# Optimization experiments

Hardware: AMD Instinct MI355X
Metric: run time of the kernel (lower is better)

Reference implementation:

```python
import jax, jax.numpy as jnp
import numpy as np

NP_CONST = 48.0  # Np in the original code


def dft_matrices(freq=48, time=512):
    # A[t, f] = exp(-2j*pi*t*f/time)/sqrt(time), split into re/im, shape [time, freq]
    t = np.arange(time)[:, None]
    f = np.arange(freq)[None, :]
    ang = -2.0 * np.pi * t * f / time
    scale = 1.0 / np.sqrt(time)
    return (np.cos(ang) * scale).astype(np.float32), (np.sin(ang) * scale).astype(np.float32)


def _mm(xr, xi, wr, wi):
    # complex matmul: (xr + i xi) @ (wr + i wi)
    return xr @ wr - xi @ wi, xr @ wi + xi @ wr


def _act(R, sigma, theta):
    # scaled soft-threshold (standard LAMP shrinkage); returns f and df/dR
    lam = theta[0] * sigma
    mag = jnp.abs(R)
    shr = jnp.maximum(mag - lam, 0.0)
    f = theta[1] * jnp.sign(R) * shr
    df = theta[1] * (mag > lam).astype(R.dtype)
    return f, df


def setup_inputs() -> dict:
    key = jax.random.key(0)
    L, B = 8, 8192
    dre, dim = dft_matrices(48, 512)
    u = jax.random.normal(key, (B, 48, 2), dtype=jnp.float32)
    # per-layer params initialized to the DFT matrices (as in LAMP_layer.__init__)
    A_re = jnp.broadcast_to(jnp.asarray(dre), (L, 512, 48)).copy()
    A_im = jnp.broadcast_to(jnp.asarray(dim), (L, 512, 48)).copy()
    theta = jnp.broadcast_to(jnp.array([1.0, 1.0, -1.0], dtype=jnp.float32), (L, 3)).copy()
    return {"u": u, "A_re": A_re, "A_im": A_im, "theta": theta,
            "DFT_re": jnp.asarray(dre), "DFT_im": jnp.asarray(dim)}


def _lamp_forward(u, A_re, A_im, theta, DFT_re, DFT_im):
    u_re, u_im = u[:, :, 0], u[:, :, 1]          # [B, 48]
    B = u_re.shape[0]
    z_re, z_im = u_re, u_im
    H_re = jnp.zeros((B, 512), dtype=u.dtype)
    H_im = jnp.zeros((B, 512), dtype=u.dtype)

    def layer(carry, params):
        z_re, z_im, H_re, H_im = carry
        Are, Aim, th = params                      # [512,48], [512,48], [3]
        # Z = z @ A.T : [B,48] x [48,512]
        Z_re, Z_im = _mm(z_re, z_im, Are.T, Aim.T)
        R_re = H_re + Z_re
        R_im = H_im + Z_im
        sigma = jnp.sqrt(jnp.sum(z_re * z_re) + jnp.sum(z_im * z_im)) / jnp.sqrt(NP_CONST)
        Hn_re, d_re = _act(R_re, sigma, th)
        Hn_im, d_im = _act(R_im, sigma, th)
        b_re = d_re.sum() / NP_CONST
        b_im = d_im.sum() / NP_CONST
        # h_hat = H_hat @ A : [B,512] x [512,48]
        h_re, h_im = _mm(Hn_re, Hn_im, Are, Aim)
        zn_re = u_re - h_re + b_re * z_re
        zn_im = u_im - h_im + b_im * z_im
        return (zn_re, zn_im, Hn_re, Hn_im), None

    (z_re, z_im, H_re, H_im), _ = jax.lax.scan(layer, (z_re, z_im, H_re, H_im),
                                               (A_re, A_im, theta))
    h_re, h_im = _mm(H_re, H_im, DFT_re, DFT_im)   # [B, 48]
    return jnp.stack((h_re, h_im), axis=2)          # [B, 48, 2]


def reference(u, A_re, A_im, theta, DFT_re, DFT_im):
    return _lamp_forward(u, A_re, A_im, theta, DFT_re, DFT_im)
```

## Files before the change

kernel.cpp:

```cpp
#include <hip/hip_runtime.h>
#include <hip/hip_bf16.h>
#include <math.h>

#define B_   8192
#define F_   48
#define T_   512
#define L_   8
#define NBLK 256
#define THR  512
#define NW   8
#define RPB  32
#define HST  520
#define ZS   52
#define LINE 32
#define EVT_DW (NBLK * LINE)
#define NEVT 8
#define SYNC_DW (NEVT * EVT_DW)

typedef unsigned short ushort_t;
typedef unsigned int   uint_t;
typedef __attribute__((ext_vector_type(8))) short short8;
typedef __attribute__((ext_vector_type(4))) float f32x4;

#define MFMA(a,b,c) __builtin_amdgcn_mfma_f32_16x16x32_bf16(a,b,c,0,0,0)

__device__ inline ushort_t f2bf(float x) {
    __hip_bfloat16 h = __float2bfloat16(x);
    return *reinterpret_cast<ushort_t*>(&h);
}
__device__ inline short8 negbf(short8 v) {
    short8 r;
    #pragma unroll
    for (int i = 0; i < 8; ++i) r[i] = v[i] ^ (short)0x8000;
    return r;
}
__device__ inline short8 pack8(float4 a, float4 b) {
    short8 r;
    r[0]=(short)f2bf(a.x); r[1]=(short)f2bf(a.y); r[2]=(short)f2bf(a.z); r[3]=(short)f2bf(a.w);
    r[4]=(short)f2bf(b.x); r[5]=(short)f2bf(b.y); r[6]=(short)f2bf(b.z); r[7]=(short)f2bf(b.w);
    return r;
}

__device__ inline float aload(const float* p) {
    return __hip_atomic_load(p, __ATOMIC_RELAXED, __HIP_MEMORY_SCOPE_AGENT);
}
__device__ inline void astore(float* p, float v) {
    __hip_atomic_store(p, v, __ATOMIC_RELAXED, __HIP_MEMORY_SCOPE_AGENT);
}

__device__ inline void publish(float* evtbase, int blk, const float* v, int nv) {
    float* line = evtbase + (size_t)blk * LINE;
    #pragma unroll
    for (int j = 0; j < 8; ++j)
        if (j < nv) astore(line + 1 + j, v[j]);
    __hip_atomic_store((uint_t*)line, 1u, __ATOMIC_RELEASE, __HIP_MEMORY_SCOPE_AGENT);
}

__device__ inline void evt_wait(float* evtbase, int wave, int lane, int nv, float* red) {
    if (wave == 0) {
        uint_t* f0 = (uint_t*)evtbase;
        for (;;) {
            bool ok = true;
            #pragma unroll
            for (int g = 0; g < NBLK / 64; ++g) {
                uint_t fl = __hip_atomic_load(f0 + (size_t)(g * 64 + lane) * LINE,
                                              __ATOMIC_RELAXED, __HIP_MEMORY_SCOPE_AGENT);
                ok = ok && (fl != 0u);
            }
            if (__all(ok)) break;
            __builtin_amdgcn_s_sleep(1);
        }
    }
    __syncthreads();
    if (wave < nv) {
        float s = 0.f;
        #pragma unroll
        for (int g = 0; g < NBLK / 64; ++g)
            s += aload(evtbase + (size_t)(g * 64 + lane) * LINE + 1 + wave);
        #pragma unroll
        for (int o = 32; o > 0; o >>= 1) s += __shfl_xor(s, o, 64);
        if (lane == 0) red[wave] = s;
    }
    __syncthreads();
}

__global__ __launch_bounds__(256) void k_pre(
    const float* __restrict__ Ar, const float* __restrict__ Ai,
    const float* __restrict__ Dr, const float* __restrict__ Di,
    ushort_t* __restrict__ Afr, ushort_t* __restrict__ Afi,
    ushort_t* __restrict__ Atr, ushort_t* __restrict__ Ati,
    ushort_t* __restrict__ Dfr, ushort_t* __restrict__ Dfi,
    uint_t* __restrict__ syncbuf)
{
    const int gt = blockIdx.x * 256 + threadIdx.x;
    const int gs = gridDim.x * 256;
    for (int idx = gt; idx < SYNC_DW; idx += gs) syncbuf[idx] = 0u;
    for (int idx = gt; idx < L_ * 32768; idx += gs) {
        int j = idx & 7, rest = idx >> 3;
        int mm = rest & 15; rest >>= 4;
        int qq = rest & 3;  rest >>= 2;
        int k2 = rest & 1;  rest >>= 1;
        int tile = rest & 31;
        int l = rest >> 5;
        int t = tile * 16 + mm, k = k2 * 32 + qq * 8 + j;
        float vr = 0.f, vi = 0.f;
        if (k < 48) { int g = l * 24576 + t * 48 + k; vr = Ar[g]; vi = Ai[g]; }
        Afr[idx] = f2bf(vr); Afi[idx] = f2bf(vi);
    }
    for (int idx = gt; idx < L_ * 24576; idx += gs) {
        int j = idx & 7, rest = idx >> 3;
        int mm = rest & 15; rest >>= 4;
        int qq = rest & 3;  rest >>= 2;
        int ks = rest & 15; rest >>= 4;
        int ft = rest % 3;
        int l = rest / 3;
        int f = ft * 16 + mm, k = ks * 32 + qq * 8 + j;
        int g = l * 24576 + k * 48 + f;
        Atr[idx] = f2bf(Ar[g]); Ati[idx] = f2bf(Ai[g]);
    }
    for (int idx = gt; idx < 24576; idx += gs) {
        int j = idx & 7, rest = idx >> 3;
        int mm = rest & 15; rest >>= 4;
        int qq = rest & 3;  rest >>= 2;
        int ks = rest & 15;
        int ft = rest >> 4;
        int f = ft * 16 + mm, k = ks * 32 + qq * 8 + j;
        Dfr[idx] = f2bf(Dr[k * 48 + f]); Dfi[idx] = f2bf(Di[k * 48 + f]);
    }
}

__global__ __launch_bounds__(THR, 2) void k_lamp(
    const float* __restrict__ u,
    const ushort_t* __restrict__ Afr, const ushort_t* __restrict__ Afi,
    const ushort_t* __restrict__ Atr, const ushort_t* __restrict__ Ati,
    const ushort_t* __restrict__ Dfr, const ushort_t* __restrict__ Dfi,
    const float* __restrict__ th,
    uint_t* syncbuf,
    float* __restrict__ out)
{
    extern __shared__ char dyn[];
    float*    pR   = (float*)dyn;
    float*    pI   = pR + 8 * 3 * 16 * 17;
    float*    zreL = pI + 8 * 3 * 16 * 17;
    float*    zimL = zreL + RPB * ZS;
    float*    red  = zimL + RPB * ZS;
    ushort_t* HreL = (ushort_t*)(red + 128);
    ushort_t* HimL = HreL + RPB * HST;

    float* evt = (float*)syncbuf;

    const int tid = threadIdx.x, blk = blockIdx.x;
    const int row0 = blk * RPB;
    const int wave = tid >> 6, lane = tid & 63;
    const int quad = lane >> 4, m = lane & 15;
    const int rows16 = (wave >> 2) * 16;
    const int rt = wave >> 2, kq = wave & 3;
    const float2* u2 = (const float2*)u;

    f32x4 hR[8], hI[8];
    #pragma unroll
    for (int ct = 0; ct < 8; ++ct) { hR[ct] = (f32x4){0,0,0,0}; hI[ct] = (f32x4){0,0,0,0}; }

    float acc = 0.f;
    #pragma unroll
    for (int k3 = 0; k3 < 3; ++k3) {
        int j = tid + k3 * THR;
        int r = j / 48, c = j - r * 48;
        float2 v = u2[(row0 + r) * 48 + c];
        zreL[r * ZS + c] = v.x; zimL[r * ZS + c] = v.y;
        acc += v.x * v.x + v.y * v.y;
    }
    #pragma unroll
    for (int o = 32; o > 0; o >>= 1) acc += __shfl_xor(acc, o, 64);
    __syncthreads();
    if (lane == 0) red[16 + wave] = acc;
    __syncthreads();
    if (tid == 0) {
        float t = 0.f;
        #pragma unroll
        for (int w = 0; w < NW; ++w) t += red[16 + w];
        publish(evt, blk, &t, 1);
    }

    float lam = 0.f;
    for (int l = 0; l < L_; ++l) {
        const float th1 = th[l * 3 + 1];

        const float* zpr = zreL + (rows16 + m) * ZS;
        const float* zpi = zimL + (rows16 + m) * ZS;
        short8 zr0 = pack8(*(const float4*)(zpr + quad * 8), *(const float4*)(zpr + quad * 8 + 4));
        short8 zi0 = pack8(*(const float4*)(zpi + quad * 8), *(const float4*)(zpi + quad * 8 + 4));
        short8 zr1 = {0,0,0,0,0,0,0,0}, zi1 = {0,0,0,0,0,0,0,0};
        if (quad < 2) {
            zr1 = pack8(*(const float4*)(zpr + 32 + quad * 8), *(const float4*)(zpr + 36 + quad * 8));
            zi1 = pack8(*(const float4*)(zpi + 32 + quad * 8), *(const float4*)(zpi + 36 + quad * 8));
        }
        short8 zin0 = negbf(zi0), zin1 = negbf(zi1);

        const ushort_t* Aflr = Afr + (size_t)l * 32768;
        const ushort_t* Afli = Afi + (size_t)l * 32768;
        #pragma unroll
        for (int ct = 0; ct < 8; ++ct) {
            const int tile = (wave & 3) * 8 + ct;
            const ushort_t* rp = Aflr + (size_t)(tile * 2) * 512 + lane * 8;
            const ushort_t* ip = Afli + (size_t)(tile * 2) * 512 + lane * 8;
            short8 ar0 = *(const short8*)rp;
            short8 ar1 = *(const short8*)(rp + 512);
            short8 ai0 = *(const short8*)ip;
            short8 ai1 = *(const short8*)(ip + 512);
            hR[ct] = MFMA(zr0, ar0, hR[ct]);
            hR[ct] = MFMA(zr1, ar1, hR[ct]);
            hR[ct] = MFMA(zin0, ai0, hR[ct]);
            hR[ct] = MFMA(zin1, ai1, hR[ct]);
            hI[ct] = MFMA(zr0, ai0, hI[ct]);
            hI[ct] = MFMA(zr1, ai1, hI[ct]);
            hI[ct] = MFMA(zi0, ar0, hI[ct]);
            hI[ct] = MFMA(zi1, ar1, hI[ct]);
        }

        if (l == 0) {
            evt_wait(evt, wave, lane, 1, red);
            lam = th[0] * sqrtf(red[0] * (1.0f / 48.0f));
        }

        float cr = 0.f, ci = 0.f;
        #pragma unroll
        for (int ct = 0; ct < 8; ++ct) {
            const int t = ((wave & 3) * 8 + ct) * 16 + m;
            #pragma unroll
            for (int reg = 0; reg < 4; ++reg) {
                const int lr = rows16 + quad * 4 + reg;
                float Rr = hR[ct][reg], Ri = hI[ct][reg];
                float mr = fabsf(Rr), mi = fabsf(Ri);
                float fr = th1 * copysignf(fmaxf(mr - lam, 0.f), Rr);
                float fi = th1 * copysignf(fmaxf(mi - lam, 0.f), Ri);
                cr += (mr > lam) ? 1.f : 0.f;
                ci += (mi > lam) ? 1.f : 0.f;
                hR[ct][reg] = fr; hI[ct][reg] = fi;
                HreL[lr * HST + t] = f2bf(fr);
                HimL[lr * HST + t] = f2bf(fi);
            }
        }

        if (l == L_ - 1) { __syncthreads(); break; }
        __syncthreads();

        const ushort_t* Atlr = Atr + (size_t)l * 24576;
        const ushort_t* Atli = Ati + (size_t)l * 24576;
        f32x4 aR[3], aI[3];
        #pragma unroll
        for (int q = 0; q < 3; ++q) { aR[q] = (f32x4){0,0,0,0}; aI[q] = (f32x4){0,0,0,0}; }
        #pragma unroll
        for (int ks = 0; ks < 4; ++ks) {
            const int ksa = kq * 4 + ks;
            const int k0 = ksa * 32 + quad * 8;
            short8 hr = *(const short8*)&HreL[(rt * 16 + m) * HST + k0];
            short8 hi = *(const short8*)&HimL[(rt * 16 + m) * HST + k0];
            short8 hin = negbf(hi);
            #pragma unroll
            for (int ft = 0; ft < 3; ++ft) {
                short8 br = *(const short8*)(Atlr + (size_t)((ft * 16 + ksa) * 64 + lane) * 8);
                short8 bi = *(const short8*)(Atli + (size_t)((ft * 16 + ksa) * 64 + lane) * 8);
                aR[ft] = MFMA(hr, br, aR[ft]);
                aR[ft] = MFMA(hin, bi, aR[ft]);
                aI[ft] = MFMA(hr, bi, aI[ft]);
                aI[ft] = MFMA(hi, br, aI[ft]);
            }
        }
        #pragma unroll
        for (int ft = 0; ft < 3; ++ft) {
            #pragma unroll
            for (int reg = 0; reg < 4; ++reg) {
                pR[((wave * 3 + ft) * 16 + quad * 4 + reg) * 17 + m] = aR[ft][reg];
                pI[((wave * 3 + ft) * 16 + quad * 4 + reg) * 17 + m] = aI[ft][reg];
            }
        }
        __syncthreads();

        float aRe[3], aIm[3], zR3[3], zI3[3];
        float S1 = 0.f, S2 = 0.f, S3 = 0.f, S4 = 0.f, S5 = 0.f, S6 = 0.f;
        #pragma unroll
        for (int k3 = 0; k3 < 3; ++k3) {
            int j = tid + k3 * THR;
            int r = j / 48, f = j - r * 48;
            int rt2 = r >> 4, lr = r & 15, ft = f >> 4, c = f & 15;
            float hRv = 0.f, hIv = 0.f;
            #pragma unroll
            for (int q = 0; q < 4; ++q) {
                hRv += pR[(((rt2 * 4 + q) * 3 + ft) * 16 + lr) * 17 + c];
                hIv += pI[(((rt2 * 4 + q) * 3 + ft) * 16 + lr) * 17 + c];
            }
            float2 uv = u2[(row0 + r) * 48 + f];
            float zr = zreL[r * ZS + f], zi = zimL[r * ZS + f];
            float ar = uv.x - hRv, ai = uv.y - hIv;
            aRe[k3] = ar; aIm[k3] = ai; zR3[k3] = zr; zI3[k3] = zi;
            S1 += ar * ar; S2 += ar * zr; S3 += zr * zr;
            S4 += ai * ai; S5 += ai * zi; S6 += zi * zi;
        }

        float v8[8] = {cr, ci, S1, S2, S3, S4, S5, S6};
        #pragma unroll
        for (int j = 0; j < 8; ++j) {
            #pragma unroll
            for (int o = 32; o > 0; o >>= 1) v8[j] += __shfl_xor(v8[j], o, 64);
        }
        if (lane == 0) {
            #pragma unroll
            for (int j = 0; j < 8; ++j) red[16 + wave * 8 + j] = v8[j];
        }
        __syncthreads();
        if (tid == 0) {
            float o8[8];
            #pragma unroll
            for (int j = 0; j < 8; ++j) {
                float s = 0.f;
                #pragma unroll
                for (int w = 0; w < NW; ++w) s += red[16 + w * 8 + j];
                o8[j] = s;
            }
            publish(evt + (size_t)(l + 1) * EVT_DW, blk, o8, 8);
        }

        evt_wait(evt + (size_t)(l + 1) * EVT_DW, wave, lane, 8, red);
        const float CR = red[0], CI = red[1];
        const float G1 = red[2], G2 = red[3], G3 = red[4];
        const float G4 = red[5], G5 = red[6], G6 = red[7];
        const float bre = th1 * CR * (1.0f / 48.0f);
        const float bim = th1 * CI * (1.0f / 48.0f);
        const float sig2 = G1 + 2.f * bre * G2 + bre * bre * G3
                         + G4 + 2.f * bim * G5 + bim * bim * G6;
        lam = th[(l + 1) * 3] * sqrtf(sig2 * (1.0f / 48.0f));

        #pragma unroll
        for (int k3 = 0; k3 < 3; ++k3) {
            int j = tid + k3 * THR;
            int r = j / 48, f = j - r * 48;
            zreL[r * ZS + f] = aRe[k3] + bre * zR3[k3];
            zimL[r * ZS + f] = aIm[k3] + bim * zI3[k3];
        }
        __syncthreads();
    }

    f32x4 fR[3], fI[3];
    #pragma unroll
    for (int q = 0; q < 3; ++q) { fR[q] = (f32x4){0,0,0,0}; fI[q] = (f32x4){0,0,0,0}; }
    #pragma unroll
    for (int ks = 0; ks < 4; ++ks) {
        const int ksa = kq * 4 + ks;
        const int k0 = ksa * 32 + quad * 8;
        short8 hr = *(const short8*)&HreL[(rt * 16 + m) * HST + k0];
        short8 hi = *(const short8*)&HimL[(rt * 16 + m) * HST + k0];
        short8 hin = negbf(hi);
        #pragma unroll
        for (int ft = 0; ft < 3; ++ft) {
            short8 br = *(const short8*)(Dfr + (size_t)((ft * 16 + ksa) * 64 + lane) * 8);
            short8 bi = *(const short8*)(Dfi + (size_t)((ft * 16 + ksa) * 64 + lane) * 8);
            fR[ft] = MFMA(hr, br, fR[ft]);
            fR[ft] = MFMA(hin, bi, fR[ft]);
            fI[ft] = MFMA(hr, bi, fI[ft]);
            fI[ft] = MFMA(hi, br, fI[ft]);
        }
    }
    #pragma unroll
    for (int ft = 0; ft < 3; ++ft) {
        #pragma unroll
        for (int reg = 0; reg < 4; ++reg) {
            pR[((wave * 3 + ft) * 16 + quad * 4 + reg) * 17 + m] = fR[ft][reg];
            pI[((wave * 3 + ft) * 16 + quad * 4 + reg) * 17 + m] = fI[ft][reg];
        }
    }
    __syncthreads();
    float2* out2 = (float2*)out;
    #pragma unroll
    for (int k3 = 0; k3 < 3; ++k3) {
        int j = tid + k3 * THR;
        int r = j / 48, f = j - r * 48;
        int rt2 = r >> 4, lr = r & 15, ft = f >> 4, c = f & 15;
        float hRv = 0.f, hIv = 0.f;
        #pragma unroll
        for (int q = 0; q < 4; ++q) {
            hRv += pR[(((rt2 * 4 + q) * 3 + ft) * 16 + lr) * 17 + c];
            hIv += pI[(((rt2 * 4 + q) * 3 + ft) * 16 + lr) * 17 + c];
        }
        out2[(row0 + r) * 48 + f] = make_float2(hRv, hIv);
    }
}

extern "C" void kernel_launch(void* const* d_in, const int* in_sizes, int n_in,
                              void* d_out, int out_size, void* d_ws, size_t ws_size,
                              hipStream_t stream) {
    (void)in_sizes; (void)n_in; (void)out_size; (void)ws_size;
    const float* u  = (const float*)d_in[0];
    const float* Ar = (const float*)d_in[1];
    const float* Ai = (const float*)d_in[2];
    const float* th = (const float*)d_in[3];
    const float* Dr = (const float*)d_in[4];
    const float* Di = (const float*)d_in[5];
    float* out = (float*)d_out;

    char* p = (char*)d_ws;
    auto alloc = [&](size_t bytes) -> char* {
        char* r = p;
        p += (bytes + 255) & ~(size_t)255;
        return r;
    };
    uint_t*   syncbuf = (uint_t*)alloc((size_t)SYNC_DW * 4);
    ushort_t* Afr = (ushort_t*)alloc((size_t)L_ * 32768 * 2);
    ushort_t* Afi = (ushort_t*)alloc((size_t)L_ * 32768 * 2);
    ushort_t* Atr = (ushort_t*)alloc((size_t)L_ * 24576 * 2);
    ushort_t* Ati = (ushort_t*)alloc((size_t)L_ * 24576 * 2);
    ushort_t* Dfr = (ushort_t*)alloc((size_t)24576 * 2);
    ushort_t* Dfi = (ushort_t*)alloc((size_t)24576 * 2);

    k_pre<<<1024, 256, 0, stream>>>(Ar, Ai, Dr, Di, Afr, Afi, Atr, Ati, Dfr, Dfi, syncbuf);

    const uint_t lds_bytes = 132608;
    hipFuncSetAttribute((const void*)k_lamp,
                        hipFuncAttributeMaxDynamicSharedMemorySize, (int)lds_bytes);
    void* args[] = { (void*)&u, (void*)&Afr, (void*)&Afi, (void*)&Atr, (void*)&Ati,
                     (void*)&Dfr, (void*)&Dfi, (void*)&th,
                     (void*)&syncbuf, (void*)&out };
    hipLaunchCooperativeKernel((void*)k_lamp, dim3(NBLK), dim3(THR), args,
                               lds_bytes, stream);
}
```

Before: 307.7 us.

## Replace per-block flag polling grid barrier with atomic-add counter and reductions

The grid-wide reduction no longer has each block write its own line while wave 0 polls all 256 flags and then sums 256 entries. Each block now atomically adds its partial sums into 4-way striped accumulators and bumps one monotonic counter, and a single thread spins on that counter and sums the 4 stripes. This cuts polling traffic and the reduction work after the barrier. In exchange, float atomics add contention on a few cache lines and make the summation order nondeterministic.

Measured after the change: 286.3 us. 7.0% less time.

```diff
diff --git a/kernel.cpp b/kernel.cpp
--- a/kernel.cpp
+++ b/kernel.cpp
@@ -13,9 +13,9 @@
 #define HST  520
 #define ZS   52
 #define LINE 32
-#define EVT_DW (NBLK * LINE)
+#define EVT_LINES 32
 #define NEVT 8
-#define SYNC_DW (NEVT * EVT_DW)
+#define SYNC_DW ((1 + NEVT * EVT_LINES) * LINE)
 
 typedef unsigned short ushort_t;
 typedef unsigned int   uint_t;
@@ -44,44 +44,30 @@
 __device__ inline float aload(const float* p) {
     return __hip_atomic_load(p, __ATOMIC_RELAXED, __HIP_MEMORY_SCOPE_AGENT);
 }
-__device__ inline void astore(float* p, float v) {
-    __hip_atomic_store(p, v, __ATOMIC_RELAXED, __HIP_MEMORY_SCOPE_AGENT);
-}
-
-__device__ inline void publish(float* evtbase, int blk, const float* v, int nv) {
-    float* line = evtbase + (size_t)blk * LINE;
-    #pragma unroll
-    for (int j = 0; j < 8; ++j)
-        if (j < nv) astore(line + 1 + j, v[j]);
-    __hip_atomic_store((uint_t*)line, 1u, __ATOMIC_RELEASE, __HIP_MEMORY_SCOPE_AGENT);
-}
-
-__device__ inline void evt_wait(float* evtbase, int wave, int lane, int nv, float* red) {
-    if (wave == 0) {
-        uint_t* f0 = (uint_t*)evtbase;
-        for (;;) {
-            bool ok = true;
-            #pragma unroll
-            for (int g = 0; g < NBLK / 64; ++g) {
-                uint_t fl = __hip_atomic_load(f0 + (size_t)(g * 64 + lane) * LINE,
-                                              __ATOMIC_RELAXED, __HIP_MEMORY_SCOPE_AGENT);
-                ok = ok && (fl != 0u);
-            }
-            if (__all(ok)) break;
-            __builtin_amdgcn_s_sleep(1);
-        }
-    }
-    __syncthreads();
-    if (wave < nv) {
+__device__ inline void afadd(float* p, float v) {
+    (void)__hip_atomic_fetch_add(p, v, __ATOMIC_RELAXED, __HIP_MEMORY_SCOPE_AGENT);
+}
+
+template<int NV>
+__device__ inline void evt_publish(float* vbase, uint_t* cnt, int blk, const float* v) {
+    #pragma unroll
+    for (int j = 0; j < NV; ++j)
+        afadd(vbase + (j * 4 + (blk & 3)) * LINE, v[j]);
+    (void)__hip_atomic_fetch_add(cnt, 1u, __ATOMIC_RELEASE, __HIP_MEMORY_SCOPE_AGENT);
+}
+
+template<int NV>
+__device__ inline void evt_consume(float* vbase, uint_t* cnt, uint_t tgt, float* red) {
+    while (__hip_atomic_load(cnt, __ATOMIC_RELAXED, __HIP_MEMORY_SCOPE_AGENT) < tgt)
+        __builtin_amdgcn_s_sleep(2);
+    (void)__hip_atomic_load(cnt, __ATOMIC_ACQUIRE, __HIP_MEMORY_SCOPE_AGENT);
+    #pragma unroll
+    for (int j = 0; j < NV; ++j) {
         float s = 0.f;
         #pragma unroll
-        for (int g = 0; g < NBLK / 64; ++g)
-            s += aload(evtbase + (size_t)(g * 64 + lane) * LINE + 1 + wave);
-        #pragma unroll
-        for (int o = 32; o > 0; o >>= 1) s += __shfl_xor(s, o, 64);
-        if (lane == 0) red[wave] = s;
-    }
-    __syncthreads();
+        for (int q = 0; q < 4; ++q) s += aload(vbase + (j * 4 + q) * LINE);
+        red[j] = s;
+    }
 }
 
 __global__ __launch_bounds__(256) void k_pre(
@@ -147,7 +133,9 @@
     ushort_t* HreL = (ushort_t*)(red + 128);
     ushort_t* HimL = HreL + RPB * HST;
 
-    float* evt = (float*)syncbuf;
+    uint_t* cnt = syncbuf;
+    float*  ev0 = (float*)syncbuf + (size_t)1 * LINE;
+    auto evb = [&](int e) { return ev0 + (size_t)e * EVT_LINES * LINE; };
 
     const int tid = threadIdx.x, blk = blockIdx.x;
     const int row0 = blk * RPB;
@@ -179,7 +167,7 @@
         float t = 0.f;
         #pragma unroll
         for (int w = 0; w < NW; ++w) t += red[16 + w];
-        publish(evt, blk, &t, 1);
+        evt_publish<1>(evb(0), cnt, blk, &t);
     }
 
     float lam = 0.f;
@@ -219,7 +207,8 @@
         }
 
         if (l == 0) {
-            evt_wait(evt, wave, lane, 1, red);
+            if (tid == 0) evt_consume<1>(evb(0), cnt, (uint_t)NBLK, red);
+            __syncthreads();
             lam = th[0] * sqrtf(red[0] * (1.0f / 48.0f));
         }
 
@@ -318,10 +307,12 @@
                 for (int w = 0; w < NW; ++w) s += red[16 + w * 8 + j];
                 o8[j] = s;
             }
-            publish(evt + (size_t)(l + 1) * EVT_DW, blk, o8, 8);
-        }
-
-        evt_wait(evt + (size_t)(l + 1) * EVT_DW, wave, lane, 8, red);
+            float* vb = evb(l + 1);
+            evt_publish<8>(vb, cnt, blk, o8);
+            evt_consume<8>(vb, cnt, (uint_t)NBLK * (uint_t)(l + 2), red);
+        }
+        __syncthreads();
+
         const float CR = red[0], CI = red[1];
         const float G1 = red[2], G2 = red[3], G3 = red[4];
         const float G4 = red[5], G5 = red[6], G6 = red[7];
```

## Split grid barrier and overlap b reduction with second matmul using counter sync

Applied to the files above, without the earlier changes.

Replaces the per-event flag polling over 256 lines with a single monotonically increasing atomic counter, and splits each layer's grid-wide reduction into two events. The onsager sums (cr, ci) are published before the second matmul and consumed after it, which hides that barrier's latency behind the MFMA work. The sigma sums are consumed at the start of the next layer instead of at the end of the current one. It also keeps u in registers instead of reloading it, zeroes only the counter in the prep kernel, halves the prep grid, and switches from a cooperative launch to a plain launch. That last change risks deadlock if all 256 blocks are not co-resident, and the single shared counter becomes a contention point for the atomics.

After: 270.5 us. -12.1%, faster.

```diff
diff --git a/kernel.cpp b/kernel.cpp
--- a/kernel.cpp
+++ b/kernel.cpp
@@ -13,9 +13,9 @@
 #define HST  520
 #define ZS   52
 #define LINE 32
-#define EVT_DW (NBLK * LINE)
-#define NEVT 8
-#define SYNC_DW (NEVT * EVT_DW)
+#define NEVT 15
+#define SLOT_DW (NBLK * LINE)
+#define SYNC_DW ((1 + NEVT * NBLK) * LINE)
 
 typedef unsigned short ushort_t;
 typedef unsigned int   uint_t;
@@ -46,42 +46,6 @@
 }
 __device__ inline void astore(float* p, float v) {
     __hip_atomic_store(p, v, __ATOMIC_RELAXED, __HIP_MEMORY_SCOPE_AGENT);
-}
-
-__device__ inline void publish(float* evtbase, int blk, const float* v, int nv) {
-    float* line = evtbase + (size_t)blk * LINE;
-    #pragma unroll
-    for (int j = 0; j < 8; ++j)
-        if (j < nv) astore(line + 1 + j, v[j]);
-    __hip_atomic_store((uint_t*)line, 1u, __ATOMIC_RELEASE, __HIP_MEMORY_SCOPE_AGENT);
-}
-
-__device__ inline void evt_wait(float* evtbase, int wave, int lane, int nv, float* red) {
-    if (wave == 0) {
-        uint_t* f0 = (uint_t*)evtbase;
-        for (;;) {
-            bool ok = true;
-            #pragma unroll
-            for (int g = 0; g < NBLK / 64; ++g) {
-                uint_t fl = __hip_atomic_load(f0 + (size_t)(g * 64 + lane) * LINE,
-                                              __ATOMIC_RELAXED, __HIP_MEMORY_SCOPE_AGENT);
-                ok = ok && (fl != 0u);
-            }
-            if (__all(ok)) break;
-            __builtin_amdgcn_s_sleep(1);
-        }
-    }
-    __syncthreads();
-    if (wave < nv) {
-        float s = 0.f;
-        #pragma unroll
-        for (int g = 0; g < NBLK / 64; ++g)
-            s += aload(evtbase + (size_t)(g * 64 + lane) * LINE + 1 + wave);
-        #pragma unroll
-        for (int o = 32; o > 0; o >>= 1) s += __shfl_xor(s, o, 64);
-        if (lane == 0) red[wave] = s;
-    }
-    __syncthreads();
 }
 
 __global__ __launch_bounds__(256) void k_pre(
@@ -94,7 +58,7 @@
 {
     const int gt = blockIdx.x * 256 + threadIdx.x;
     const int gs = gridDim.x * 256;
-    for (int idx = gt; idx < SYNC_DW; idx += gs) syncbuf[idx] = 0u;
+    if (gt < LINE) syncbuf[gt] = 0u;
     for (int idx = gt; idx < L_ * 32768; idx += gs) {
         int j = idx & 7, rest = idx >> 3;
         int mm = rest & 15; rest >>= 4;
@@ -147,7 +111,8 @@
     ushort_t* HreL = (ushort_t*)(red + 128);
     ushort_t* HimL = HreL + RPB * HST;
 
-    float* evt = (float*)syncbuf;
+    uint_t* cnt   = syncbuf;
+    float*  slots = (float*)syncbuf + LINE;
 
     const int tid = threadIdx.x, blk = blockIdx.x;
     const int row0 = blk * RPB;
@@ -157,16 +122,49 @@
     const int rt = wave >> 2, kq = wave & 3;
     const float2* u2 = (const float2*)u;
 
+    auto publishv = [&](int e, const float* v, int nv) {
+        float* line = slots + (size_t)e * SLOT_DW + (size_t)blk * LINE;
+        for (int j = 0; j < nv; ++j) astore(line + j, v[j]);
+        (void)__hip_atomic_fetch_add(cnt, 1u, __ATOMIC_RELEASE,
+                                     __HIP_MEMORY_SCOPE_AGENT);
+    };
+    auto consume = [&](int e, int nv) {
+        if (tid == 0) {
+            uint_t tgt = (uint_t)NBLK * (uint_t)(e + 1);
+            int spin = 0;
+            while (__hip_atomic_load(cnt, __ATOMIC_RELAXED,
+                                     __HIP_MEMORY_SCOPE_AGENT) < tgt) {
+                if (++spin > 2) __builtin_amdgcn_s_sleep(8);
+            }
+            (void)__hip_atomic_load(cnt, __ATOMIC_ACQUIRE,
+                                    __HIP_MEMORY_SCOPE_AGENT);
+        }
+        __syncthreads();
+        if (wave < nv) {
+            const float* base = slots + (size_t)e * SLOT_DW;
+            float s = 0.f;
+            #pragma unroll
+            for (int g = 0; g < 4; ++g)
+                s += aload(base + (size_t)(g * 64 + lane) * LINE + wave);
+            #pragma unroll
+            for (int o = 32; o > 0; o >>= 1) s += __shfl_xor(s, o, 64);
+            if (lane == 0) red[wave] = s;
+        }
+        __syncthreads();
+    };
+
     f32x4 hR[8], hI[8];
     #pragma unroll
     for (int ct = 0; ct < 8; ++ct) { hR[ct] = (f32x4){0,0,0,0}; hI[ct] = (f32x4){0,0,0,0}; }
 
+    float uRe[3], uIm[3];
     float acc = 0.f;
     #pragma unroll
     for (int k3 = 0; k3 < 3; ++k3) {
         int j = tid + k3 * THR;
         int r = j / 48, c = j - r * 48;
         float2 v = u2[(row0 + r) * 48 + c];
+        uRe[k3] = v.x; uIm[k3] = v.y;
         zreL[r * ZS + c] = v.x; zimL[r * ZS + c] = v.y;
         acc += v.x * v.x + v.y * v.y;
     }
@@ -179,10 +177,10 @@
         float t = 0.f;
         #pragma unroll
         for (int w = 0; w < NW; ++w) t += red[16 + w];
-        publish(evt, blk, &t, 1);
-    }
-
-    float lam = 0.f;
+        publishv(0, &t, 1);
+    }
+
+    float lam = 0.f, bre = 0.f, bim = 0.f;
     for (int l = 0; l < L_; ++l) {
         const float th1 = th[l * 3 + 1];
 
@@ -219,8 +217,13 @@
         }
 
         if (l == 0) {
-            evt_wait(evt, wave, lane, 1, red);
+            consume(0, 1);
             lam = th[0] * sqrtf(red[0] * (1.0f / 48.0f));
+        } else {
+            consume(2 * l, 6);
+            float sig2 = red[0] + 2.f * bre * red[1] + bre * bre * red[2]
+                       + red[3] + 2.f * bim * red[4] + bim * bim * red[5];
+            lam = th[l * 3] * sqrtf(sig2 * (1.0f / 48.0f));
         }
 
         float cr = 0.f, ci = 0.f;
@@ -243,7 +246,17 @@
         }
 
         if (l == L_ - 1) { __syncthreads(); break; }
-        __syncthreads();
+
+        #pragma unroll
+        for (int o = 32; o > 0; o >>= 1) { cr += __shfl_xor(cr, o, 64); ci += __shfl_xor(ci, o, 64); }
+        if (lane == 0) { red[16 + wave] = cr; red[24 + wave] = ci; }
+        __syncthreads();
+        if (tid == 0) {
+            float v2[2] = {0.f, 0.f};
+            #pragma unroll
+            for (int w = 0; w < NW; ++w) { v2[0] += red[16 + w]; v2[1] += red[24 + w]; }
+            publishv(2 * l + 1, v2, 2);
+        }
 
         const ushort_t* Atlr = Atr + (size_t)l * 24576;
         const ushort_t* Atli = Ati + (size_t)l * 24576;
@@ -277,6 +290,10 @@
         }
         __syncthreads();
 
+        consume(2 * l + 1, 2);
+        bre = th1 * red[0] * (1.0f / 48.0f);
+        bim = th1 * red[1] * (1.0f / 48.0f);
+
         float aRe[3], aIm[3], zR3[3], zI3[3];
         float S1 = 0.f, S2 = 0.f, S3 = 0.f, S4 = 0.f, S5 = 0.f, S6 = 0.f;
         #pragma unroll
@@ -290,46 +307,35 @@
                 hRv += pR[(((rt2 * 4 + q) * 3 + ft) * 16 + lr) * 17 + c];
                 hIv += pI[(((rt2 * 4 + q) * 3 + ft) * 16 + lr) * 17 + c];
             }
-            float2 uv = u2[(row0 + r) * 48 + f];
             float zr = zreL[r * ZS + f], zi = zimL[r * ZS + f];
-            float ar = uv.x - hRv, ai = uv.y - hIv;
+            float ar = uRe[k3] - hRv, ai = uIm[k3] - hIv;
             aRe[k3] = ar; aIm[k3] = ai; zR3[k3] = zr; zI3[k3] = zi;
             S1 += ar * ar; S2 += ar * zr; S3 += zr * zr;
             S4 += ai * ai; S5 += ai * zi; S6 += zi * zi;
         }
 
-        float v8[8] = {cr, ci, S1, S2, S3, S4, S5, S6};
-        #pragma unroll
-        for (int j = 0; j < 8; ++j) {
-            #pragma unroll
-            for (int o = 32; o > 0; o >>= 1) v8[j] += __shfl_xor(v8[j], o, 64);
+        float v6[6] = {S1, S2, S3, S4, S5, S6};
+        #pragma unroll
+        for (int j = 0; j < 6; ++j) {
+            #pragma unroll
+            for (int o = 32; o > 0; o >>= 1) v6[j] += __shfl_xor(v6[j], o, 64);
         }
         if (lane == 0) {
             #pragma unroll
-            for (int j = 0; j < 8; ++j) red[16 + wave * 8 + j] = v8[j];
+            for (int j = 0; j < 6; ++j) red[16 + wave * 6 + j] = v6[j];
         }
         __syncthreads();
         if (tid == 0) {
-            float o8[8];
-            #pragma unroll
-            for (int j = 0; j < 8; ++j) {
+            float o6[6];
+            #pragma unroll
+            for (int j = 0; j < 6; ++j) {
                 float s = 0.f;
                 #pragma unroll
-                for (int w = 0; w < NW; ++w) s += red[16 + w * 8 + j];
-                o8[j] = s;
-            }
-            publish(evt + (size_t)(l + 1) * EVT_DW, blk, o8, 8);
-        }
-
-        evt_wait(evt + (size_t)(l + 1) * EVT_DW, wave, lane, 8, red);
-        const float CR = red[0], CI = red[1];
-        const float G1 = red[2], G2 = red[3], G3 = red[4];
-        const float G4 = red[5], G5 = red[6], G6 = red[7];
-        const float bre = th1 * CR * (1.0f / 48.0f);
-        const float bim = th1 * CI * (1.0f / 48.0f);
-        const float sig2 = G1 + 2.f * bre * G2 + bre * bre * G3
-                         + G4 + 2.f * bim * G5 + bim * bim * G6;
-        lam = th[(l + 1) * 3] * sqrtf(sig2 * (1.0f / 48.0f));
+                for (int w = 0; w < NW; ++w) s += red[16 + w * 6 + j];
+                o6[j] = s;
+            }
+            publishv(2 * l + 2, o6, 6);
+        }
 
         #pragma unroll
         for (int k3 = 0; k3 < 3; ++k3) {
@@ -412,14 +418,11 @@
     ushort_t* Dfr = (ushort_t*)alloc((size_t)24576 * 2);
     ushort_t* Dfi = (ushort_t*)alloc((size_t)24576 * 2);
 
-    k_pre<<<1024, 256, 0, stream>>>(Ar, Ai, Dr, Di, Afr, Afi, Atr, Ati, Dfr, Dfi, syncbuf);
+    k_pre<<<512, 256, 0, stream>>>(Ar, Ai, Dr, Di, Afr, Afi, Atr, Ati, Dfr, Dfi, syncbuf);
 
     const uint_t lds_bytes = 132608;
     hipFuncSetAttribute((const void*)k_lamp,
                         hipFuncAttributeMaxDynamicSharedMemorySize, (int)lds_bytes);
-    void* args[] = { (void*)&u, (void*)&Afr, (void*)&Afi, (void*)&Atr, (void*)&Ati,
-                     (void*)&Dfr, (void*)&Dfi, (void*)&th,
-                     (void*)&syncbuf, (void*)&out };
-    hipLaunchCooperativeKernel((void*)k_lamp, dim3(NBLK), dim3(THR), args,
-                               lds_bytes, stream);
-}
+    k_lamp<<<dim3(NBLK), dim3(THR), lds_bytes, stream>>>(
+        u, Afr, Afi, Atr, Ati, Dfr, Dfi, th, syncbuf, out);
+}
```
